# Performance work log

Hardware: AMD Instinct MI355X
Metric: run time of the kernel (lower is better)

## Reference

```python
import jax, jax.numpy as jnp
import numpy as np

ALPHA = 300.0  # attractor strength (exp variant: exp(-alpha*|dx|^gamma)*dx, gamma=2)


def setup_inputs() -> dict:
    key = jax.random.key(0)
    k0, k1, k2, k3 = jax.random.split(key, 4)
    n, c, h, w = 4, 256, 128, 128
    mlp_dim, n_attractors, n_bins = 128, 16, 64
    x = jax.random.normal(k0, (n, c, h, w), jnp.float32)
    b_prev = jax.random.uniform(k1, (n, n_bins, h, w), jnp.float32)  # bin centers
    w1 = jax.random.normal(k2, (mlp_dim, c), jnp.float32) * 0.02
    b1 = jnp.zeros((mlp_dim,), jnp.float32)
    w2 = jax.random.normal(k3, (n_attractors, mlp_dim), jnp.float32) * 0.02
    b2 = jnp.zeros((n_attractors,), jnp.float32)
    return {"x": x, "b_prev": b_prev, "w1": w1, "b1": b1, "w2": w2, "b2": b2}


def reference(x, b_prev, w1, b1, w2, b2):
    # 1x1 conv MLP head: Conv2d(c->mlp) -> ReLU -> Conv2d(mlp->n_attractors) -> Softplus
    hfeat = jax.nn.relu(jnp.einsum('nchw,oc->nohw', x, w1) + b1[None, :, None, None])
    A = jax.nn.softplus(jnp.einsum('nchw,oc->nohw', hfeat, w2) + b2[None, :, None, None])
    # b_prev interpolated to (h, w) == identity here (same spatial size)
    b_centers = b_prev
    # dx: [n, n_attractors, n_bins, h, w]
    dx = A[:, :, None, :, :] - b_centers[:, None, :, :, :]
    # exp attractor with gamma=2: exp(-alpha*dx^2) * dx, summed over attractors ('sum' kind)
    delta_c = jnp.sum(jnp.exp(-ALPHA * dx * dx) * dx, axis=1)
    b_new_centers = b_centers + delta_c
    return (b_new_centers, b_new_centers)
```

## Files before the change

### kernel.cpp

```cpp
#include <hip/hip_runtime.h>
#include <hip/hip_bf16.h>
#include <stdint.h>


#define HW 16384
#define ALPHA 300.0f

typedef short bf16x8_t __attribute__((ext_vector_type(8)));
typedef float f32x4_t __attribute__((ext_vector_type(4)));
typedef unsigned int u32x4_t __attribute__((ext_vector_type(4)));

__device__ __forceinline__ unsigned short f2bf(float f) {
  unsigned int u = __builtin_bit_cast(unsigned int, f);
  u += 0x7fffu + ((u >> 16) & 1u);
  return (unsigned short)(u >> 16);
}
__device__ __forceinline__ unsigned int pack2(float a, float b) {
  return (unsigned int)f2bf(a) | ((unsigned int)f2bf(b) << 16);
}
__device__ __forceinline__ float ald(const float* p) {
  float r;
  asm volatile("global_load_dword %0, %1, off" : "=v"(r) : "v"(p));
  return r;
}
__device__ __forceinline__ u32x4_t ald4(const void* p) {
  u32x4_t r;
  asm volatile("global_load_dwordx4 %0, %1, off" : "=v"(r) : "v"(p));
  return r;
}

__global__ void zoed_prep(const float* __restrict__ w1,
                          const float* __restrict__ w2,
                          unsigned short* __restrict__ blob) {
  int i = blockIdx.x * 256 + threadIdx.x;
  if (i < 32768) {
    int o = i >> 8, c = i & 255;
    float v = w1[i];
    int idx = (c >> 5) * 4096 + o * 32 + ((((c >> 3) & 3) ^ (o & 3)) << 3) + (c & 7);
    blob[idx] = f2bf(v);
  } else {
    int i2 = i - 32768;
    int a = i2 >> 7, o = i2 & 127;
    float v = w2[i2];
    int idx = 32768 + (o >> 5) * 512 + a * 32 + ((((o >> 3) & 3) ^ (a & 3)) << 3) + (o & 7);
    blob[idx] = f2bf(v);
  }
}

#define KITER(KB, NWAIT, AFNEXT, XNEXT)                                     \
  {                                                                         \
    constexpr int kb = KB;                                                  \
    if (AFNEXT) {                                                           \
      _Pragma("unroll") for (int tm = 0; tm < 8; tm++)                      \
          af[(kb + 1) & 1][tm] = ald4(wb + (kb + 1) * 8192 + tm * 1024);    \
    }                                                                       \
    if (XNEXT) {                                                            \
      _Pragma("unroll") for (int j = 0; j < 8; j++)                         \
          xr[(kb + 3) & 3][j] = ald(xb + (size_t)((kb + 3) * 32 + j) * HW); \
    }                                                                       \
    asm volatile("s_waitcnt vmcnt(" #NWAIT ")");                            \
    __builtin_amdgcn_sched_barrier(0);                                      \
    u32x4_t v = {pack2(xr[kb & 3][0], xr[kb & 3][1]),                       \
                 pack2(xr[kb & 3][2], xr[kb & 3][3]),                       \
                 pack2(xr[kb & 3][4], xr[kb & 3][5]),                       \
                 pack2(xr[kb & 3][6], xr[kb & 3][7])};                      \
    bf16x8_t bfm = __builtin_bit_cast(bf16x8_t, v);                         \
    _Pragma("unroll") for (int tm = 0; tm < 8; tm++)                        \
        acc[tm] = __builtin_amdgcn_mfma_f32_16x16x32_bf16(                  \
            __builtin_bit_cast(bf16x8_t, af[kb & 1][tm]), bfm, acc[tm], 0,  \
            0, 0);                                                          \
  }

__global__ __launch_bounds__(256, 3) void zoed_fused(
    const float* __restrict__ x, const float* __restrict__ bprev,
    const float* __restrict__ b1, const float* __restrict__ b2,
    const unsigned short* __restrict__ wblob, float* __restrict__ out) {
  __shared__ __align__(16) char smem[21504];

  const int t = threadIdx.x;
  const int lane = t & 63;
  const int l15 = lane & 15;
  const int quad = lane >> 4;
  const int wv = t >> 6;
  const int sw = ((quad ^ (l15 & 3)) << 4);

  const int blk = blockIdx.x;
  const int n = blk >> 8;
  const int p0 = ((blk & 255) << 6) + wv * 16;

  char* hid = smem + wv * 4096;
  char* Ab = smem + 16384 + wv * 1280;

  const float* xb = x + (size_t)(n * 256 + quad * 8) * HW + p0 + l15;
  const char* wb = (const char*)wblob + l15 * 64 + sw;

  u32x4_t af[2][8];
#pragma unroll
  for (int tm = 0; tm < 8; tm++) af[0][tm] = ald4(wb + tm * 1024);
  float xr[4][8];
#pragma unroll
  for (int c = 0; c < 3; c++)
#pragma unroll
    for (int j = 0; j < 8; j++)
      xr[c][j] = ald(xb + (size_t)(c * 32 + j) * HW);

  f32x4_t acc[8];
#pragma unroll
  for (int i = 0; i < 8; i++) acc[i] = (f32x4_t){0.f, 0.f, 0.f, 0.f};

  KITER(0, 32, 1, 1)
  KITER(1, 24, 1, 1)
  KITER(2, 24, 1, 1)
  KITER(3, 24, 1, 1)
  KITER(4, 24, 1, 1)
  KITER(5, 16, 1, 0)
  KITER(6, 8, 1, 0)
  KITER(7, 0, 0, 0)

  size_t obase = (size_t)(n * 64 + quad * 16) * HW + p0 + l15;
  const float* bp = bprev + obase;
  float bpr[16];
#pragma unroll
  for (int b = 0; b < 16; b++) bpr[b] = bp[(size_t)b * HW];
  bf16x8_t a2[4];
#pragma unroll
  for (int kc = 0; kc < 4; kc++)
    a2[kc] = *(const bf16x8_t*)((const char*)wblob + 65536 + kc * 1024 +
                                l15 * 64 + sw);

#pragma unroll
  for (int tm = 0; tm < 8; tm++) {
    f32x4_t b1v = *(const f32x4_t*)(b1 + tm * 16 + quad * 4);
    f32x4_t h = acc[tm] + b1v;
    h[0] = fmaxf(h[0], 0.f);
    h[1] = fmaxf(h[1], 0.f);
    h[2] = fmaxf(h[2], 0.f);
    h[3] = fmaxf(h[3], 0.f);
    int kc = tm >> 1;
    int g = (tm & 1) * 2 + (quad >> 1);
    int off8 = (quad & 1) * 8;
    unsigned int* dst = (unsigned int*)(hid + kc * 1024 + l15 * 64 +
                                        ((g ^ (l15 & 3)) << 4) + off8);
    dst[0] = pack2(h[0], h[1]);
    dst[1] = pack2(h[2], h[3]);
  }
  f32x4_t acc2 = (f32x4_t){0.f, 0.f, 0.f, 0.f};
#pragma unroll
  for (int kc = 0; kc < 4; kc++) {
    bf16x8_t bh = *(const bf16x8_t*)(hid + kc * 1024 + l15 * 64 + sw);
    acc2 = __builtin_amdgcn_mfma_f32_16x16x32_bf16(a2[kc], bh, acc2, 0, 0, 0);
  }
  {
    f32x4_t b2v = *(const f32x4_t*)(b2 + quad * 4);
    f32x4_t z = acc2 + b2v;
    f32x4_t spv;
#pragma unroll
    for (int r = 0; r < 4; r++) {
      float zz = z[r];
      spv[r] = fmaxf(zz, 0.f) + log1pf(__expf(-fabsf(zz)));
    }
    *(f32x4_t*)(Ab + l15 * 80 + quad * 16) = spv;
  }
  float Av[16];
#pragma unroll
  for (int r = 0; r < 4; r++) {
    f32x4_t v = *(const f32x4_t*)(Ab + l15 * 80 + r * 16);
    Av[r * 4 + 0] = v[0];
    Av[r * 4 + 1] = v[1];
    Av[r * 4 + 2] = v[2];
    Av[r * 4 + 3] = v[3];
  }
  float* o1 = out + obase;
  float* o2 = o1 + (size_t)256 * HW;
#pragma unroll
  for (int b = 0; b < 16; b++) {
    float c = bpr[b];
    float d0 = 0.f, d1 = 0.f;
#pragma unroll
    for (int a = 0; a < 8; a++) {
      float dx = Av[a] - c;
      float e = __expf(dx * dx * -ALPHA);
      d0 = fmaf(e, dx, d0);
    }
#pragma unroll
    for (int a = 8; a < 16; a++) {
      float dx = Av[a] - c;
      float e = __expf(dx * dx * -ALPHA);
      d1 = fmaf(e, dx, d1);
    }
    float r = c + (d0 + d1);
    __builtin_nontemporal_store(r, o1 + (size_t)b * HW);
    __builtin_nontemporal_store(r, o2 + (size_t)b * HW);
  }
}

extern "C" void kernel_launch(void* const* d_in, const int* in_sizes, int n_in,
                              void* d_out, int out_size, void* d_ws,
                              size_t ws_size, hipStream_t stream) {
  const float* x = (const float*)d_in[0];
  const float* bprev = (const float*)d_in[1];
  const float* w1 = (const float*)d_in[2];
  const float* b1 = (const float*)d_in[3];
  const float* w2 = (const float*)d_in[4];
  const float* b2 = (const float*)d_in[5];
  float* outp = (float*)d_out;
  unsigned short* blob = (unsigned short*)d_ws;

  zoed_prep<<<136, 256, 0, stream>>>(w1, w2, blob);
  zoed_fused<<<1024, 256, 0, stream>>>(x, bprev, b1, b2, blob, outp);
}
```

Baseline: 140.9 us.

## Single-buffer weight fragments, use hardware bf16 pack, exp2, and SGPR-based loads

Moves the MFMA block ahead of the next-stage loads so the weight fragment array can be single-buffered, which cuts register use and lets occupancy rise to 4 blocks per CU. The software bf16 rounding is replaced with v_cvt_pk_bf16_f32. Global loads now take an SGPR base plus a 32-bit VGPR offset, which saves address VGPRs. The attractor loop uses packed float2 arithmetic with a direct v_exp_f32 and a prescaled log2 constant. Issuing loads after compute shortens the prefetch distance, so memory latency may be less well hidden.

Result: no change. 141.2 us (+0.2%).

```diff
diff --git a/kernel.cpp b/kernel.cpp
--- a/kernel.cpp
+++ b/kernel.cpp
@@ -5,9 +5,11 @@
 
 #define HW 16384
 #define ALPHA 300.0f
+#define EXP2K -432.8085122666891f
 
 typedef short bf16x8_t __attribute__((ext_vector_type(8)));
 typedef float f32x4_t __attribute__((ext_vector_type(4)));
+typedef float f32x2_t __attribute__((ext_vector_type(2)));
 typedef unsigned int u32x4_t __attribute__((ext_vector_type(4)));
 
 __device__ __forceinline__ unsigned short f2bf(float f) {
@@ -15,17 +17,24 @@
   u += 0x7fffu + ((u >> 16) & 1u);
   return (unsigned short)(u >> 16);
 }
-__device__ __forceinline__ unsigned int pack2(float a, float b) {
-  return (unsigned int)f2bf(a) | ((unsigned int)f2bf(b) << 16);
-}
-__device__ __forceinline__ float ald(const float* p) {
+__device__ __forceinline__ unsigned int cvtpk(float lo, float hi) {
+  unsigned int r;
+  asm("v_cvt_pk_bf16_f32 %0, %1, %2" : "=v"(r) : "v"(lo), "v"(hi));
+  return r;
+}
+__device__ __forceinline__ float exp2a(float x) {
   float r;
-  asm volatile("global_load_dword %0, %1, off" : "=v"(r) : "v"(p));
-  return r;
-}
-__device__ __forceinline__ u32x4_t ald4(const void* p) {
+  asm("v_exp_f32 %0, %1" : "=v"(r) : "v"(x));
+  return r;
+}
+__device__ __forceinline__ float aldo(unsigned int voff, const void* sbase) {
+  float r;
+  asm volatile("global_load_dword %0, %1, %2" : "=v"(r) : "v"(voff), "s"(sbase));
+  return r;
+}
+__device__ __forceinline__ u32x4_t ald4o(unsigned int voff, const void* sbase) {
   u32x4_t r;
-  asm volatile("global_load_dwordx4 %0, %1, off" : "=v"(r) : "v"(p));
+  asm volatile("global_load_dwordx4 %0, %1, %2" : "=v"(r) : "v"(voff), "s"(sbase));
   return r;
 }
 
@@ -50,28 +59,30 @@
 #define KITER(KB, NWAIT, AFNEXT, XNEXT)                                     \
   {                                                                         \
     constexpr int kb = KB;                                                  \
+    asm volatile("s_waitcnt vmcnt(" #NWAIT ")");                            \
+    __builtin_amdgcn_sched_barrier(0);                                      \
+    u32x4_t v = {cvtpk(xr[kb & 3][0], xr[kb & 3][1]),                       \
+                 cvtpk(xr[kb & 3][2], xr[kb & 3][3]),                       \
+                 cvtpk(xr[kb & 3][4], xr[kb & 3][5]),                       \
+                 cvtpk(xr[kb & 3][6], xr[kb & 3][7])};                      \
+    bf16x8_t bfm = __builtin_bit_cast(bf16x8_t, v);                         \
+    _Pragma("unroll") for (int tm = 0; tm < 8; tm++)                        \
+        acc[tm] = __builtin_amdgcn_mfma_f32_16x16x32_bf16(                  \
+            __builtin_bit_cast(bf16x8_t, af[tm]), bfm, acc[tm], 0, 0, 0);   \
+    __builtin_amdgcn_sched_barrier(0);                                      \
     if (AFNEXT) {                                                           \
       _Pragma("unroll") for (int tm = 0; tm < 8; tm++)                      \
-          af[(kb + 1) & 1][tm] = ald4(wb + (kb + 1) * 8192 + tm * 1024);    \
+          af[tm] =                                                          \
+              ald4o(voffw + (unsigned)((kb + 1) * 8192 + tm * 1024), wblob);\
     }                                                                       \
     if (XNEXT) {                                                            \
       _Pragma("unroll") for (int j = 0; j < 8; j++)                         \
-          xr[(kb + 3) & 3][j] = ald(xb + (size_t)((kb + 3) * 32 + j) * HW); \
+          xr[(kb + 3) & 3][j] =                                             \
+              aldo(voffx + (unsigned)(((kb + 3) * 32 + j) * HW) * 4u, xs);  \
     }                                                                       \
-    asm volatile("s_waitcnt vmcnt(" #NWAIT ")");                            \
-    __builtin_amdgcn_sched_barrier(0);                                      \
-    u32x4_t v = {pack2(xr[kb & 3][0], xr[kb & 3][1]),                       \
-                 pack2(xr[kb & 3][2], xr[kb & 3][3]),                       \
-                 pack2(xr[kb & 3][4], xr[kb & 3][5]),                       \
-                 pack2(xr[kb & 3][6], xr[kb & 3][7])};                      \
-    bf16x8_t bfm = __builtin_bit_cast(bf16x8_t, v);                         \
-    _Pragma("unroll") for (int tm = 0; tm < 8; tm++)                        \
-        acc[tm] = __builtin_amdgcn_mfma_f32_16x16x32_bf16(                  \
-            __builtin_bit_cast(bf16x8_t, af[kb & 1][tm]), bfm, acc[tm], 0,  \
-            0, 0);                                                          \
-  }
-
-__global__ __launch_bounds__(256, 3) void zoed_fused(
+  }
+
+__global__ __launch_bounds__(256, 4) void zoed_fused(
     const float* __restrict__ x, const float* __restrict__ bprev,
     const float* __restrict__ b1, const float* __restrict__ b2,
     const unsigned short* __restrict__ wblob, float* __restrict__ out) {
@@ -91,30 +102,31 @@
   char* hid = smem + wv * 4096;
   char* Ab = smem + 16384 + wv * 1280;
 
-  const float* xb = x + (size_t)(n * 256 + quad * 8) * HW + p0 + l15;
-  const char* wb = (const char*)wblob + l15 * 64 + sw;
-
-  u32x4_t af[2][8];
-#pragma unroll
-  for (int tm = 0; tm < 8; tm++) af[0][tm] = ald4(wb + tm * 1024);
+  const float* xs = x + (size_t)(n * 256) * HW;
+  const unsigned voffx = (unsigned)((quad * 8) * HW + p0 + l15) * 4u;
+  const unsigned voffw = (unsigned)(l15 * 64 + sw);
+
+  u32x4_t af[8];
+#pragma unroll
+  for (int tm = 0; tm < 8; tm++) af[tm] = ald4o(voffw + tm * 1024, wblob);
   float xr[4][8];
 #pragma unroll
   for (int c = 0; c < 3; c++)
 #pragma unroll
     for (int j = 0; j < 8; j++)
-      xr[c][j] = ald(xb + (size_t)(c * 32 + j) * HW);
+      xr[c][j] = aldo(voffx + (unsigned)((c * 32 + j) * HW) * 4u, xs);
 
   f32x4_t acc[8];
 #pragma unroll
   for (int i = 0; i < 8; i++) acc[i] = (f32x4_t){0.f, 0.f, 0.f, 0.f};
 
-  KITER(0, 32, 1, 1)
-  KITER(1, 24, 1, 1)
-  KITER(2, 24, 1, 1)
-  KITER(3, 24, 1, 1)
-  KITER(4, 24, 1, 1)
-  KITER(5, 16, 1, 0)
-  KITER(6, 8, 1, 0)
+  KITER(0, 16, 1, 1)
+  KITER(1, 8, 1, 1)
+  KITER(2, 8, 1, 1)
+  KITER(3, 8, 1, 1)
+  KITER(4, 8, 1, 1)
+  KITER(5, 8, 1, 0)
+  KITER(6, 0, 1, 0)
   KITER(7, 0, 0, 0)
 
   size_t obase = (size_t)(n * 64 + quad * 16) * HW + p0 + l15;
@@ -141,8 +153,8 @@
     int off8 = (quad & 1) * 8;
     unsigned int* dst = (unsigned int*)(hid + kc * 1024 + l15 * 64 +
                                         ((g ^ (l15 & 3)) << 4) + off8);
-    dst[0] = pack2(h[0], h[1]);
-    dst[1] = pack2(h[2], h[3]);
+    dst[0] = cvtpk(h[0], h[1]);
+    dst[1] = cvtpk(h[2], h[3]);
   }
   f32x4_t acc2 = (f32x4_t){0.f, 0.f, 0.f, 0.f};
 #pragma unroll
@@ -161,34 +173,39 @@
     }
     *(f32x4_t*)(Ab + l15 * 80 + quad * 16) = spv;
   }
-  float Av[16];
-#pragma unroll
-  for (int r = 0; r < 4; r++) {
-    f32x4_t v = *(const f32x4_t*)(Ab + l15 * 80 + r * 16);
-    Av[r * 4 + 0] = v[0];
-    Av[r * 4 + 1] = v[1];
-    Av[r * 4 + 2] = v[2];
-    Av[r * 4 + 3] = v[3];
-  }
+  f32x2_t av2[8];
+#pragma unroll
+  for (int q = 0; q < 4; q++) {
+    f32x4_t v = *(const f32x4_t*)(Ab + l15 * 80 + q * 16);
+    av2[q * 2] = (f32x2_t){v[0], v[1]};
+    av2[q * 2 + 1] = (f32x2_t){v[2], v[3]};
+  }
+  const f32x2_t K2 = {EXP2K, EXP2K};
   float* o1 = out + obase;
   float* o2 = o1 + (size_t)256 * HW;
 #pragma unroll
   for (int b = 0; b < 16; b++) {
     float c = bpr[b];
-    float d0 = 0.f, d1 = 0.f;
-#pragma unroll
-    for (int a = 0; a < 8; a++) {
-      float dx = Av[a] - c;
-      float e = __expf(dx * dx * -ALPHA);
-      d0 = fmaf(e, dx, d0);
+    f32x2_t c2 = {c, c};
+    f32x2_t d0 = {0.f, 0.f}, d1 = {0.f, 0.f};
+#pragma unroll
+    for (int k = 0; k < 4; k++) {
+      f32x2_t dx = av2[k] - c2;
+      f32x2_t tt = dx * K2;
+      f32x2_t arg = tt * dx;
+      f32x2_t e = {exp2a(arg[0]), exp2a(arg[1])};
+      d0 = e * dx + d0;
     }
 #pragma unroll
-    for (int a = 8; a < 16; a++) {
-      float dx = Av[a] - c;
-      float e = __expf(dx * dx * -ALPHA);
-      d1 = fmaf(e, dx, d1);
+    for (int k = 4; k < 8; k++) {
+      f32x2_t dx = av2[k] - c2;
+      f32x2_t tt = dx * K2;
+      f32x2_t arg = tt * dx;
+      f32x2_t e = {exp2a(arg[0]), exp2a(arg[1])};
+      d1 = e * dx + d1;
     }
-    float r = c + (d0 + d1);
+    f32x2_t ds = d0 + d1;
+    float r = c + (ds[0] + ds[1]);
     __builtin_nontemporal_store(r, o1 + (size_t)b * HW);
     __builtin_nontemporal_store(r, o2 + (size_t)b * HW);
   }
```
